# Optimization experiments

Hardware: AMD Instinct MI355X
Metric: run time of the kernel (lower is better)

The kernel has to match this reference:

```python
import jax, jax.numpy as jnp
import numpy as np

C = 640      # in_channels == out_channels (required by source: same generator applied to both)
K = 3        # kernel_size
R = int(C * 0.2)  # reduction hidden = 128
H = 10
W = 10
BS = 25      # support: 5-way 5-shot
BQ = 75      # query: 5-way 15-query


def setup_inputs() -> dict:
    key = jax.random.key(0)
    ks = jax.random.split(key, 16)
    s = 0.02  # weight scale to keep the 4-deep linear chain numerically tame
    rn = lambda k, shape: jax.random.normal(k, shape, jnp.float32) * s
    return {
        "support_set": jax.random.normal(ks[0], (BS, C, H, W), jnp.float32),
        "query_set": jax.random.normal(ks[1], (BQ, C, H, W), jnp.float32),
        # ContextLearningModule: four 1x1 convs (no nonlinearity in source)
        "Wc1": rn(ks[2], (C, C)), "bc1": jnp.zeros((C,), jnp.float32),
        "Wc2": rn(ks[3], (C, C)), "bc2": jnp.zeros((C,), jnp.float32),
        "Wc3": rn(ks[4], (C, C)), "bc3": jnp.zeros((C,), jnp.float32),
        "Wc4": rn(ks[5], (C, C)), "bc4": jnp.zeros((C,), jnp.float32),
        # DynamicKernelGenerator channel branch: Linear(C,R) -> ReLU -> Linear(R, C*K*K)
        "W1": rn(ks[6], (C, R)), "b1": jnp.zeros((R,), jnp.float32),
        "W2": rn(ks[7], (R, C * K * K)), "b2": jnp.zeros((C * K * K,), jnp.float32),
        # DynamicKernelGenerator spatial branch: Conv2d(C, K*K, 1)
        "Ws": rn(ks[8], (K * K, C)), "bs": jnp.zeros((K * K,), jnp.float32),
    }


def _conv1x1(x, Wt, b):
    # x: [b, c, h, w], Wt: [o, c]
    return jnp.einsum('bchw,oc->bohw', x, Wt) + b[None, :, None, None]


def _dyn_kernel(x, W1, b1, W2, b2, Ws, bs):
    # x: [b, C, h, w] -> per-pixel dynamic kernel [b, C, h, w, K, K]
    b, c, h, w = x.shape
    pooled = x.mean(axis=(2, 3))  # adaptive_avg_pool2d(...,1)
    ck = jax.nn.relu(pooled @ W1 + b1) @ W2 + b2          # [b, C*K*K]
    ck = ck.reshape(b, c, K, K)                            # channel kernel
    sk = jnp.einsum('bchw,kc->bkhw', x, Ws) + bs[None, :, None, None]
    sk = sk.reshape(b, h, w, K, K)                         # raw view, as in source
    return ck[:, :, None, None, :, :] * sk[:, None, :, :, :, :]


def _involution(x, kernel):
    # x: [b, C, h, w]; kernel: [b or 1, C, h, w, K, K]
    # out[b,c,i,j] = sum_{u,v} kernel[b,c,i,j,u,v] * x[b,c,i+u-p, j+v-p]
    h, w = x.shape[-2:]
    p = K // 2
    xp = jnp.pad(x, ((0, 0), (0, 0), (p, p), (p, p)))
    return sum(kernel[..., u, v] * xp[:, :, u:u + h, v:v + w]
               for u in range(K) for v in range(K))


def reference(support_set, query_set, Wc1, bc1, Wc2, bc2, Wc3, bc3, Wc4, bc4,
              W1, b1, W2, b2, Ws, bs):
    sf, qf = support_set, query_set  # identity backbone
    # context learning module
    tsr = _conv1x1(_conv1x1(_conv1x1(_conv1x1(sf, Wc1, bc1), Wc2, bc2), Wc3, bc3), Wc4, bc4)
    # task-specific kernel, averaged over the support batch -> [1, C, H, W, K, K]
    task_kernel = _dyn_kernel(tsr, W1, b1, W2, b2, Ws, bs).mean(axis=0, keepdims=True)
    # per-instance kernels (batched; identical math to the per-sample loop)
    inst_kernels = _dyn_kernel(sf, W1, b1, W2, b2, Ws, bs)  # [BS, C, H, W, K, K]
    fused = inst_kernels * task_kernel
    adapted_support = _involution(sf, fused)        # [BS, C, H, W]
    adapted_query = _involution(qf, task_kernel)    # [BQ, C, H, W] (kernel broadcast)
    return (adapted_support, adapted_query)
```

## Files before the change

kernel.cpp:

```cpp
#include <hip/hip_runtime.h>

#define CCH   640
#define RDIM  128
#define HWPIX 100
#define NBS   25
#define NBQ   75
#define CKK   5760
#define SF_B  64000

#define OFF_PG0   0
#define OFF_PGA   16000
#define OFF_PGB   32000
#define OFF_ATA   48000
#define OFF_ATB   53760
#define OFF_BA    59520
#define OFF_BB    59536
#define OFF_HP    59552
#define OFF_SKT   85152
#define OFF_SKS   130152
#define OFF_SKSCT 175152
#define OFF_CKT   197652
#define OFF_CKS   341652
#define OFF_TASKT 485652

__global__ void pool_kernel(const float* __restrict__ sf, float* __restrict__ Pg0) {
    int idx = blockIdx.x * 64 + threadIdx.x;
    if (idx >= NBS * CCH) return;
    int b = idx / CCH, c = idx % CCH;
    const float4* s4 = (const float4*)(sf + b * SF_B + c * HWPIX);
    float acc = 0.f;
#pragma unroll
    for (int q = 0; q < 25; ++q) {
        float4 v = s4[q];
        acc += (v.x + v.y) + (v.z + v.w);
    }
    Pg0[idx] = acc * 0.01f;
}

__global__ void chain_step(const float* __restrict__ Pin, const float* __restrict__ Wp,
                           const float* __restrict__ bp, float* __restrict__ Pout,
                           const float* __restrict__ Ain, const float* __restrict__ Wa,
                           const float* __restrict__ ba, const float* __restrict__ Bin,
                           float* __restrict__ Aout, float* __restrict__ Bout,
                           int first, const float* __restrict__ Ws, const float* __restrict__ bs) {
    __shared__ float red[256];
    int blk = blockIdx.x, t = threadIdx.x;
    int lane = t & 63;
    if (blk < 4000) {
        int W = blk * 4 + (t >> 6);
        int o = W / NBS, b = W % NBS;
        const float2* w2 = (const float2*)(Wp + o * CCH);
        const float2* p2 = (const float2*)(Pin + b * CCH);
        float acc = 0.f;
#pragma unroll
        for (int s = 0; s < 5; ++s) {
            float2 wv = w2[s * 64 + lane];
            float2 pv = p2[s * 64 + lane];
            acc += wv.x * pv.x + wv.y * pv.y;
        }
#pragma unroll
        for (int m = 32; m >= 1; m >>= 1) acc += __shfl_xor(acc, m);
        if (lane == 0) Pout[b * CCH + o] = acc + bp[o];
    } else if (blk < 4090) {
        int w = blk - 4000;
        int k = w / 10, ctile = w % 10;
        int og = t >> 6, cl = lane;
        int c = ctile * 64 + cl;
        int o0 = og * 160;
        float acc = 0.f;
        if (first) {
            const float* ar = Ws + k * CCH;
#pragma unroll 8
            for (int o = o0; o < o0 + 160; ++o)
                acc += ar[o] * Wa[o * CCH + c];
        } else {
#pragma unroll 8
            for (int o = o0; o < o0 + 160; ++o)
                acc += Ain[o * 9 + k] * Wa[o * CCH + c];
        }
        red[t] = acc;
        __syncthreads();
        if (t < 64) {
            float s = red[t] + red[64 + t] + red[128 + t] + red[192 + t];
            Aout[(ctile * 64 + t) * 9 + k] = s;
        }
    } else {
        int WB = (blk - 4090) * 4 + (t >> 6);
        if (WB >= 9) return;
        int k = WB;
        float acc = 0.f;
        if (first) {
            const float* ar = Ws + k * CCH;
#pragma unroll
            for (int s = 0; s < 10; ++s) acc += ar[s * 64 + lane] * ba[s * 64 + lane];
        } else {
#pragma unroll
            for (int s = 0; s < 10; ++s) acc += Ain[(s * 64 + lane) * 9 + k] * ba[s * 64 + lane];
        }
#pragma unroll
        for (int m = 32; m >= 1; m >>= 1) acc += __shfl_xor(acc, m);
        if (lane == 0) Bout[k] = acc + (first ? bs[k] : Bin[k]);
    }
}

__global__ void postchain(const float* __restrict__ sf, const float* __restrict__ Pg0,
                          const float* __restrict__ Pgf, const float* __restrict__ W1,
                          float* __restrict__ Hp, const float* __restrict__ A4T,
                          const float* __restrict__ betaF, const float* __restrict__ Ws,
                          const float* __restrict__ bs, float* __restrict__ SKT,
                          float* __restrict__ SKS) {
    int blk = blockIdx.x, t = threadIdx.x;
    if (blk < 100) {
        int pair = blk / 2;
        int s = (blk % 2) * 2 + (t >> 7);
        int r = t & 127;
        int branch = pair / NBS, b = pair % NBS;
        const float* prow = (branch ? Pg0 : Pgf) + b * CCH;
        int c0 = s * 160;
        float acc = 0.f;
#pragma unroll 8
        for (int c = 0; c < 160; ++c)
            acc += prow[c0 + c] * W1[(c0 + c) * RDIM + r];
        Hp[(pair * 4 + s) * RDIM + r] = acc;
    } else {
        int sidx = (blk - 100) * 256 + t;
        if (sidx >= 45000) return;
        int s = sidx / 22500;
        int rem = sidx % 22500;
        int b = rem / 900;
        int r2 = rem % 900;
        int k = r2 / HWPIX, q = r2 % HWPIX;
        const float* x = sf + b * SF_B + q;
        const float* wsr = Ws + k * CCH;
        int c0 = s * 320;
        float acc0 = 0.f, acc1 = 0.f;
#pragma unroll 8
        for (int c = 0; c < 320; ++c) {
            float xc = x[(c0 + c) * HWPIX];
            acc0 += A4T[(c0 + c) * 9 + k] * xc;
            acc1 += wsr[c0 + c] * xc;
        }
        if (s == 0) { acc0 += betaF[k]; acc1 += bs[k]; }
        int p = r2 / 9, uv = r2 % 9;
        int dst = s * 22500 + b * 900 + uv * 100 + p;
        SKT[dst] = acc0;
        SKS[dst] = acc1;
    }
}

__global__ void mlp_phase2(const float* __restrict__ Hp, const float* __restrict__ b1,
                           const float* __restrict__ W2, const float* __restrict__ b2,
                           float* __restrict__ ckt, float* __restrict__ cks) {
    __shared__ float hs0[RDIM], hs1[RDIM];
    int b = blockIdx.x / 9, chunk = blockIdx.x % 9;
    int t = threadIdx.x;
    if (t < RDIM) {
        const float* hp = Hp + b * 4 * RDIM;
        hs0[t] = fmaxf(b1[t] + hp[t] + hp[RDIM + t] + hp[2 * RDIM + t] + hp[3 * RDIM + t], 0.f);
    } else if (t < 2 * RDIM) {
        int r = t - RDIM;
        const float* hp = Hp + (NBS + b) * 4 * RDIM;
        hs1[r] = fmaxf(b1[r] + hp[r] + hp[RDIM + r] + hp[2 * RDIM + r] + hp[3 * RDIM + r], 0.f);
    }
    __syncthreads();
    int jbase = chunk * 640;
    float a00 = b2[jbase + t], a01 = b2[jbase + t + 320];
    float a10 = a00, a11 = a01;
#pragma unroll 4
    for (int r = 0; r < RDIM; ++r) {
        const float* wrow = W2 + r * CKK + jbase;
        float w0 = wrow[t], w1 = wrow[t + 320];
        float h0 = hs0[r], h1 = hs1[r];
        a00 += h0 * w0; a01 += h0 * w1;
        a10 += h1 * w0; a11 += h1 * w1;
    }
    float* c0 = ckt + b * CKK + jbase;
    float* c1 = cks + b * CKK + jbase;
    c0[t] = a00; c0[t + 320] = a01;
    c1[t] = a10; c1[t + 320] = a11;
}

__global__ void task_assemble(const float* __restrict__ ckt, const float* __restrict__ SKT,
                              const float* __restrict__ SKS, float* __restrict__ taskT,
                              float* __restrict__ sksT) {
    int blk = blockIdx.x, t = threadIdx.x;
    if (blk < 2250) {
        int idx = blk * 256 + t;
        int uv = idx / 64000;
        int rem = idx % 64000;
        int c = rem / 100, p = rem % 100;
        float acc = 0.f;
#pragma unroll
        for (int b = 0; b < NBS; ++b)
            acc += ckt[b * CKK + c * 9 + uv] *
                   (SKT[b * 900 + uv * 100 + p] + SKT[22500 + b * 900 + uv * 100 + p]);
        taskT[idx] = acc * 0.04f;
    } else {
        int cidx = (blk - 2250) * 256 + t;
        if (cidx >= 22500) return;
        int uv = cidx / 2500;
        int r = cidx % 2500;
        int src = (r / 100) * 900 + uv * 100 + (r % 100);
        sksT[cidx] = SKS[src] + SKS[22500 + src];
    }
}

__global__ __launch_bounds__(256) void involutions(
        const float* __restrict__ sf, const float* __restrict__ qf,
        const float* __restrict__ taskT, const float* __restrict__ cks,
        const float* __restrict__ sksT, float* __restrict__ out) {
    int idx = blockIdx.x * 256 + threadIdx.x;
    bool support = idx < NBS * SF_B;
    int b, c, p;
    const float* x;
    if (support) {
        b = idx / SF_B; int rem = idx % SF_B; c = rem / 100; p = rem % 100;
        x = sf + b * SF_B + c * 100;
    } else {
        int qidx = idx - NBS * SF_B;
        b = qidx / SF_B; int rem = qidx % SF_B; c = rem / 100; p = rem % 100;
        x = qf + b * SF_B + c * 100;
    }
    int i = p / 10, j = p % 10;
    float acc = 0.f;
#pragma unroll
    for (int u = 0; u < 3; ++u) {
        int ii = i + u - 1;
        float mrow = ((unsigned)ii < 10u) ? 1.f : 0.f;
        int ci = min(max(ii, 0), 9);
#pragma unroll
        for (int v = 0; v < 3; ++v) {
            int jj = j + v - 1;
            float m = ((unsigned)jj < 10u) ? mrow : 0.f;
            int cj = min(max(jj, 0), 9);
            float xv = x[ci * 10 + cj] * m;
            int uv = u * 3 + v;
            float w = taskT[uv * 64000 + c * 100 + p];
            if (support)
                w *= cks[b * CKK + c * 9 + uv] * sksT[uv * 2500 + b * 100 + p];
            acc += w * xv;
        }
    }
    out[idx] = acc;
}

extern "C" void kernel_launch(void* const* d_in, const int* in_sizes, int n_in,
                              void* d_out, int out_size, void* d_ws, size_t ws_size,
                              hipStream_t stream) {
    const float* sf  = (const float*)d_in[0];
    const float* qf  = (const float*)d_in[1];
    const float* Wc[4] = {(const float*)d_in[2], (const float*)d_in[4],
                          (const float*)d_in[6], (const float*)d_in[8]};
    const float* bc[4] = {(const float*)d_in[3], (const float*)d_in[5],
                          (const float*)d_in[7], (const float*)d_in[9]};
    const float* W1 = (const float*)d_in[10];
    const float* b1 = (const float*)d_in[11];
    const float* W2 = (const float*)d_in[12];
    const float* b2 = (const float*)d_in[13];
    const float* Ws = (const float*)d_in[14];
    const float* bs = (const float*)d_in[15];
    float* out = (float*)d_out;
    float* ws = (float*)d_ws;

    float* Pg0 = ws + OFF_PG0;
    float* Pga = ws + OFF_PGA;
    float* Pgb = ws + OFF_PGB;
    float* ATa = ws + OFF_ATA;
    float* ATb = ws + OFF_ATB;
    float* Ba  = ws + OFF_BA;
    float* Bb  = ws + OFF_BB;
    float* Hp  = ws + OFF_HP;
    float* SKT = ws + OFF_SKT;
    float* SKS = ws + OFF_SKS;
    float* SKsT= ws + OFF_SKSCT;
    float* CKT = ws + OFF_CKT;
    float* CKS = ws + OFF_CKS;
    float* TKT = ws + OFF_TASKT;

    pool_kernel<<<250, 64, 0, stream>>>(sf, Pg0);

    chain_step<<<4093, 256, 0, stream>>>(Pg0, Wc[0], bc[0], Pga, nullptr, Wc[3], bc[3], nullptr,
                                         ATa, Ba, 1, Ws, bs);
    chain_step<<<4093, 256, 0, stream>>>(Pga, Wc[1], bc[1], Pgb, ATa, Wc[2], bc[2], Ba,
                                         ATb, Bb, 0, Ws, bs);
    chain_step<<<4093, 256, 0, stream>>>(Pgb, Wc[2], bc[2], Pga, ATb, Wc[1], bc[1], Bb,
                                         ATa, Ba, 0, Ws, bs);
    chain_step<<<4093, 256, 0, stream>>>(Pga, Wc[3], bc[3], Pgb, ATa, Wc[0], bc[0], Ba,
                                         ATb, Bb, 0, Ws, bs);

    postchain<<<276, 256, 0, stream>>>(sf, Pg0, Pgb, W1, Hp, ATb, Bb, Ws, bs, SKT, SKS);
    mlp_phase2<<<225, 320, 0, stream>>>(Hp, b1, W2, b2, CKT, CKS);
    task_assemble<<<2338, 256, 0, stream>>>(CKT, SKT, SKS, TKT, SKsT);
    involutions<<<25000, 256, 0, stream>>>(sf, qf, TKT, CKS, SKsT, out);
}
```

Baseline: 234.5 us.

## Merge front-end kernels into one persistent kernel with grid barriers

Replaces the eight small launches (pool, four chain steps, postchain, MLP, task assembly) with one persistent 512-block kernel that moves between phases using atomic-counter grid barriers. It also restructures the work: the last P chain step overlaps with the spatial-kernel computation, and the MLP's first layer is recomputed per block instead of being staged through the Hp buffer. The goal is to cut launch overhead and the tails between dependent small kernels. The cost is spin-wait barriers, which deadlock if the 512 blocks are not all resident at once, plus fewer blocks for the large task-assembly phase and redundant W1 work (each of 450 blocks recomputes a full 640x128 matvec).

```diff
diff --git a/kernel.cpp b/kernel.cpp
--- a/kernel.cpp
+++ b/kernel.cpp
@@ -2,11 +2,10 @@
 
 #define CCH   640
 #define RDIM  128
-#define HWPIX 100
 #define NBS   25
-#define NBQ   75
 #define CKK   5760
 #define SF_B  64000
+#define NBLK  512
 
 #define OFF_PG0   0
 #define OFF_PGA   16000
@@ -15,193 +14,248 @@
 #define OFF_ATB   53760
 #define OFF_BA    59520
 #define OFF_BB    59536
-#define OFF_HP    59552
-#define OFF_SKT   85152
-#define OFF_SKS   130152
-#define OFF_SKSCT 175152
-#define OFF_CKT   197652
-#define OFF_CKS   341652
-#define OFF_TASKT 485652
-
-__global__ void pool_kernel(const float* __restrict__ sf, float* __restrict__ Pg0) {
-    int idx = blockIdx.x * 64 + threadIdx.x;
-    if (idx >= NBS * CCH) return;
-    int b = idx / CCH, c = idx % CCH;
-    const float4* s4 = (const float4*)(sf + b * SF_B + c * HWPIX);
-    float acc = 0.f;
+#define OFF_SKT   59552
+#define OFF_SKS   104552
+#define OFF_SKSCT 149552
+#define OFF_CKT   172052
+#define OFF_CKS   316052
+#define OFF_TASKT 460052
+#define OFF_BAR   2000000
+
+#define GSYNC(id) do {                                                        \
+    __syncthreads();                                                          \
+    if (t == 0) {                                                             \
+        __threadfence();                                                      \
+        unsigned prev_ = atomicAdd(&bar[(id)], 1u);                           \
+        if (prev_ != (unsigned)(NBLK - 1)) {                                  \
+            while (atomicAdd(&bar[(id)], 0u) < (unsigned)NBLK) {              \
+                for (volatile int z_ = 0; z_ < 128; ++z_) {}                  \
+            }                                                                 \
+        }                                                                     \
+        __threadfence();                                                      \
+    }                                                                         \
+    __syncthreads();                                                          \
+} while (0)
+
+#define P_STEP(Pin, Wp, bp, Pout, WG0, STR) do {                              \
+    for (int W_ = (WG0); W_ < 16000; W_ += (STR)) {                           \
+        int o_ = W_ / NBS, b_ = W_ % NBS;                                     \
+        const float2* w2_ = (const float2*)((Wp) + o_ * CCH);                 \
+        const float2* p2_ = (const float2*)((Pin) + b_ * CCH);                \
+        float acc_ = 0.f;                                                     \
+        for (int s_ = 0; s_ < 5; ++s_) {                                      \
+            float2 wv_ = w2_[s_ * 64 + lane];                                 \
+            float2 pv_ = p2_[s_ * 64 + lane];                                 \
+            acc_ += wv_.x * pv_.x + wv_.y * pv_.y;                            \
+        }                                                                     \
+        for (int m_ = 32; m_ >= 1; m_ >>= 1) acc_ += __shfl_xor(acc_, m_);    \
+        if (lane == 0) (Pout)[b_ * CCH + o_] = acc_ + (bp)[o_];               \
+    }                                                                         \
+} while (0)
+
+#define A_STEP(w, Ain, Wa, Aout) do {                                         \
+    int k_ = (w) / 10, ctile_ = (w) % 10;                                     \
+    int og_ = t >> 6, cl_ = t & 63;                                           \
+    int c_ = ctile_ * 64 + cl_;                                               \
+    int o0_ = og_ * 160;                                                      \
+    float acc_ = 0.f;                                                         \
+    for (int o_ = o0_; o_ < o0_ + 160; ++o_)                                  \
+        acc_ += (Ain)[o_ * 9 + k_] * (Wa)[o_ * CCH + c_];                     \
+    red[t] = acc_;                                                            \
+    __syncthreads();                                                          \
+    if (t < 64)                                                               \
+        (Aout)[(ctile_ * 64 + t) * 9 + k_] =                                  \
+            red[t] + red[64 + t] + red[128 + t] + red[192 + t];               \
+} while (0)
+
+#define A_STEP_FIRST(w, Wa, Aout) do {                                        \
+    int k_ = (w) / 10, ctile_ = (w) % 10;                                     \
+    int og_ = t >> 6, cl_ = t & 63;                                           \
+    int c_ = ctile_ * 64 + cl_;                                               \
+    int o0_ = og_ * 160;                                                      \
+    const float* ar_ = Ws + k_ * CCH;                                         \
+    float acc_ = 0.f;                                                         \
+    for (int o_ = o0_; o_ < o0_ + 160; ++o_)                                  \
+        acc_ += ar_[o_] * (Wa)[o_ * CCH + c_];                                \
+    red[t] = acc_;                                                            \
+    __syncthreads();                                                          \
+    if (t < 64)                                                               \
+        (Aout)[(ctile_ * 64 + t) * 9 + k_] =                                  \
+            red[t] + red[64 + t] + red[128 + t] + red[192 + t];               \
+} while (0)
+
+#define B_STEP(kidx, Ain, bvec, Bin, Bout) do {                               \
+    float acc_ = 0.f;                                                         \
+    for (int s_ = 0; s_ < 10; ++s_) {                                         \
+        int e_ = s_ * 64 + lane;                                              \
+        acc_ += (Ain)[e_ * 9 + (kidx)] * (bvec)[e_];                          \
+    }                                                                         \
+    for (int m_ = 32; m_ >= 1; m_ >>= 1) acc_ += __shfl_xor(acc_, m_);        \
+    if (lane == 0) (Bout)[(kidx)] = acc_ + (Bin)[(kidx)];                     \
+} while (0)
+
+#define B_STEP_FIRST(kidx, bvec, Bout) do {                                   \
+    const float* ar_ = Ws + (kidx) * CCH;                                     \
+    float acc_ = 0.f;                                                         \
+    for (int s_ = 0; s_ < 10; ++s_) {                                         \
+        int e_ = s_ * 64 + lane;                                              \
+        acc_ += ar_[e_] * (bvec)[e_];                                         \
+    }                                                                         \
+    for (int m_ = 32; m_ >= 1; m_ >>= 1) acc_ += __shfl_xor(acc_, m_);        \
+    if (lane == 0) (Bout)[(kidx)] = acc_ + bs[(kidx)];                        \
+} while (0)
+
+__global__ __launch_bounds__(256) void mega_front(
+        const float* __restrict__ sf,
+        const float* __restrict__ Wc1, const float* __restrict__ bc1,
+        const float* __restrict__ Wc2, const float* __restrict__ bc2,
+        const float* __restrict__ Wc3, const float* __restrict__ bc3,
+        const float* __restrict__ Wc4, const float* __restrict__ bc4,
+        const float* __restrict__ W1, const float* __restrict__ b1,
+        const float* __restrict__ W2, const float* __restrict__ b2,
+        const float* __restrict__ Ws, const float* __restrict__ bs,
+        float* __restrict__ ws) {
+    __shared__ float red[256];
+    const int blk = blockIdx.x, t = threadIdx.x;
+    const int lane = t & 63, wib = t >> 6;
+
+    float* Pg0 = ws + OFF_PG0;
+    float* Pga = ws + OFF_PGA;
+    float* Pgb = ws + OFF_PGB;
+    float* ATa = ws + OFF_ATA;
+    float* ATb = ws + OFF_ATB;
+    float* Ba  = ws + OFF_BA;
+    float* Bb  = ws + OFF_BB;
+    float* SKT = ws + OFF_SKT;
+    float* SKS = ws + OFF_SKS;
+    float* SKsT = ws + OFF_SKSCT;
+    float* CKT = ws + OFF_CKT;
+    float* CKS = ws + OFF_CKS;
+    float* TKT = ws + OFF_TASKT;
+    unsigned* bar = (unsigned*)(ws + OFF_BAR);
+
+    if (blk < 63) {
+        int idx = blk * 256 + t;
+        if (idx < NBS * CCH) {
+            int b = idx / CCH, c = idx % CCH;
+            const float4* s4 = (const float4*)(sf + b * SF_B + c * 100);
+            float acc = 0.f;
 #pragma unroll
-    for (int q = 0; q < 25; ++q) {
-        float4 v = s4[q];
-        acc += (v.x + v.y) + (v.z + v.w);
-    }
-    Pg0[idx] = acc * 0.01f;
-}
-
-__global__ void chain_step(const float* __restrict__ Pin, const float* __restrict__ Wp,
-                           const float* __restrict__ bp, float* __restrict__ Pout,
-                           const float* __restrict__ Ain, const float* __restrict__ Wa,
-                           const float* __restrict__ ba, const float* __restrict__ Bin,
-                           float* __restrict__ Aout, float* __restrict__ Bout,
-                           int first, const float* __restrict__ Ws, const float* __restrict__ bs) {
-    __shared__ float red[256];
-    int blk = blockIdx.x, t = threadIdx.x;
-    int lane = t & 63;
-    if (blk < 4000) {
-        int W = blk * 4 + (t >> 6);
-        int o = W / NBS, b = W % NBS;
-        const float2* w2 = (const float2*)(Wp + o * CCH);
-        const float2* p2 = (const float2*)(Pin + b * CCH);
-        float acc = 0.f;
-#pragma unroll
-        for (int s = 0; s < 5; ++s) {
-            float2 wv = w2[s * 64 + lane];
-            float2 pv = p2[s * 64 + lane];
-            acc += wv.x * pv.x + wv.y * pv.y;
-        }
-#pragma unroll
-        for (int m = 32; m >= 1; m >>= 1) acc += __shfl_xor(acc, m);
-        if (lane == 0) Pout[b * CCH + o] = acc + bp[o];
-    } else if (blk < 4090) {
-        int w = blk - 4000;
-        int k = w / 10, ctile = w % 10;
-        int og = t >> 6, cl = lane;
-        int c = ctile * 64 + cl;
-        int o0 = og * 160;
-        float acc = 0.f;
-        if (first) {
-            const float* ar = Ws + k * CCH;
+            for (int q = 0; q < 25; ++q) {
+                float4 v = s4[q];
+                acc += (v.x + v.y) + (v.z + v.w);
+            }
+            Pg0[idx] = acc * 0.01f;
+        }
+    } else if (blk < 153) {
+        A_STEP_FIRST(blk - 63, Wc4, ATa);
+    } else if (blk < 156) {
+        int kk = (blk - 153) * 4 + wib;
+        if (kk < 9) B_STEP_FIRST(kk, bc4, Ba);
+    }
+    GSYNC(0);
+
+    if (blk < 419) {
+        P_STEP(Pg0, Wc1, bc1, Pga, blk * 4 + wib, 1676);
+    } else if (blk < 509) {
+        A_STEP(blk - 419, ATa, Wc3, ATb);
+    } else {
+        int kk = (blk - 509) * 4 + wib;
+        if (kk < 9) B_STEP(kk, ATa, bc3, Ba, Bb);
+    }
+    GSYNC(1);
+
+    if (blk < 419) {
+        P_STEP(Pga, Wc2, bc2, Pgb, blk * 4 + wib, 1676);
+    } else if (blk < 509) {
+        A_STEP(blk - 419, ATb, Wc2, ATa);
+    } else {
+        int kk = (blk - 509) * 4 + wib;
+        if (kk < 9) B_STEP(kk, ATb, bc2, Bb, Ba);
+    }
+    GSYNC(2);
+
+    if (blk < 419) {
+        P_STEP(Pgb, Wc3, bc3, Pga, blk * 4 + wib, 1676);
+    } else if (blk < 509) {
+        A_STEP(blk - 419, ATa, Wc1, ATb);
+    } else {
+        int kk = (blk - 509) * 4 + wib;
+        if (kk < 9) B_STEP(kk, ATa, bc1, Ba, Bb);
+    }
+    GSYNC(3);
+
+    if (blk < 176) {
+        int sidx = blk * 256 + t;
+        if (sidx < 45000) {
+            int s = sidx / 22500;
+            int rem = sidx % 22500;
+            int b = rem / 900;
+            int r2 = rem % 900;
+            int k = r2 / 100, q = r2 % 100;
+            const float* x = sf + b * SF_B + q;
+            const float* wsr = Ws + k * CCH;
+            int c0 = s * 320;
+            float acc0 = 0.f, acc1 = 0.f;
 #pragma unroll 8
-            for (int o = o0; o < o0 + 160; ++o)
-                acc += ar[o] * Wa[o * CCH + c];
-        } else {
+            for (int c = 0; c < 320; ++c) {
+                float xc = x[(c0 + c) * 100];
+                acc0 += ATb[(c0 + c) * 9 + k] * xc;
+                acc1 += wsr[c0 + c] * xc;
+            }
+            if (s == 0) { acc0 += Bb[k]; acc1 += bs[k]; }
+            int p = r2 / 9, uv = r2 % 9;
+            int dst = s * 22500 + b * 900 + uv * 100 + p;
+            SKT[dst] = acc0;
+            SKS[dst] = acc1;
+        }
+    } else {
+        P_STEP(Pga, Wc4, bc4, Pgb, (blk - 176) * 4 + wib, 1344);
+    }
+    GSYNC(4);
+
+    if (blk < 450) {
+        int b = blk / 18, jc = blk % 18, jb = jc * 320;
+        {
+            int r = t & 127;
+            const float* prow = ((t < 128) ? Pgb : Pg0) + b * CCH;
+            float acc = b1[r];
 #pragma unroll 8
-            for (int o = o0; o < o0 + 160; ++o)
-                acc += Ain[o * 9 + k] * Wa[o * CCH + c];
-        }
-        red[t] = acc;
+            for (int c = 0; c < CCH; ++c) acc += prow[c] * W1[c * RDIM + r];
+            red[t] = fmaxf(acc, 0.f);
+        }
         __syncthreads();
-        if (t < 64) {
-            float s = red[t] + red[64 + t] + red[128 + t] + red[192 + t];
-            Aout[(ctile * 64 + t) * 9 + k] = s;
-        }
-    } else {
-        int WB = (blk - 4090) * 4 + (t >> 6);
-        if (WB >= 9) return;
-        int k = WB;
-        float acc = 0.f;
-        if (first) {
-            const float* ar = Ws + k * CCH;
-#pragma unroll
-            for (int s = 0; s < 10; ++s) acc += ar[s * 64 + lane] * ba[s * 64 + lane];
-        } else {
-#pragma unroll
-            for (int s = 0; s < 10; ++s) acc += Ain[(s * 64 + lane) * 9 + k] * ba[s * 64 + lane];
-        }
-#pragma unroll
-        for (int m = 32; m >= 1; m >>= 1) acc += __shfl_xor(acc, m);
-        if (lane == 0) Bout[k] = acc + (first ? bs[k] : Bin[k]);
-    }
-}
-
-__global__ void postchain(const float* __restrict__ sf, const float* __restrict__ Pg0,
-                          const float* __restrict__ Pgf, const float* __restrict__ W1,
-                          float* __restrict__ Hp, const float* __restrict__ A4T,
-                          const float* __restrict__ betaF, const float* __restrict__ Ws,
-                          const float* __restrict__ bs, float* __restrict__ SKT,
-                          float* __restrict__ SKS) {
-    int blk = blockIdx.x, t = threadIdx.x;
-    if (blk < 100) {
-        int pair = blk / 2;
-        int s = (blk % 2) * 2 + (t >> 7);
-        int r = t & 127;
-        int branch = pair / NBS, b = pair % NBS;
-        const float* prow = (branch ? Pg0 : Pgf) + b * CCH;
-        int c0 = s * 160;
-        float acc = 0.f;
-#pragma unroll 8
-        for (int c = 0; c < 160; ++c)
-            acc += prow[c0 + c] * W1[(c0 + c) * RDIM + r];
-        Hp[(pair * 4 + s) * RDIM + r] = acc;
-    } else {
-        int sidx = (blk - 100) * 256 + t;
-        if (sidx >= 45000) return;
-        int s = sidx / 22500;
-        int rem = sidx % 22500;
-        int b = rem / 900;
-        int r2 = rem % 900;
-        int k = r2 / HWPIX, q = r2 % HWPIX;
-        const float* x = sf + b * SF_B + q;
-        const float* wsr = Ws + k * CCH;
-        int c0 = s * 320;
-        float acc0 = 0.f, acc1 = 0.f;
-#pragma unroll 8
-        for (int c = 0; c < 320; ++c) {
-            float xc = x[(c0 + c) * HWPIX];
-            acc0 += A4T[(c0 + c) * 9 + k] * xc;
-            acc1 += wsr[c0 + c] * xc;
-        }
-        if (s == 0) { acc0 += betaF[k]; acc1 += bs[k]; }
-        int p = r2 / 9, uv = r2 % 9;
-        int dst = s * 22500 + b * 900 + uv * 100 + p;
-        SKT[dst] = acc0;
-        SKS[dst] = acc1;
-    }
-}
-
-__global__ void mlp_phase2(const float* __restrict__ Hp, const float* __restrict__ b1,
-                           const float* __restrict__ W2, const float* __restrict__ b2,
-                           float* __restrict__ ckt, float* __restrict__ cks) {
-    __shared__ float hs0[RDIM], hs1[RDIM];
-    int b = blockIdx.x / 9, chunk = blockIdx.x % 9;
-    int t = threadIdx.x;
-    if (t < RDIM) {
-        const float* hp = Hp + b * 4 * RDIM;
-        hs0[t] = fmaxf(b1[t] + hp[t] + hp[RDIM + t] + hp[2 * RDIM + t] + hp[3 * RDIM + t], 0.f);
-    } else if (t < 2 * RDIM) {
-        int r = t - RDIM;
-        const float* hp = Hp + (NBS + b) * 4 * RDIM;
-        hs1[r] = fmaxf(b1[r] + hp[r] + hp[RDIM + r] + hp[2 * RDIM + r] + hp[3 * RDIM + r], 0.f);
-    }
-    __syncthreads();
-    int jbase = chunk * 640;
-    float a00 = b2[jbase + t], a01 = b2[jbase + t + 320];
-    float a10 = a00, a11 = a01;
+        for (int j = jb + t; j < jb + 320; j += 256) {
+            float a0 = b2[j], a1 = b2[j];
 #pragma unroll 4
-    for (int r = 0; r < RDIM; ++r) {
-        const float* wrow = W2 + r * CKK + jbase;
-        float w0 = wrow[t], w1 = wrow[t + 320];
-        float h0 = hs0[r], h1 = hs1[r];
-        a00 += h0 * w0; a01 += h0 * w1;
-        a10 += h1 * w0; a11 += h1 * w1;
-    }
-    float* c0 = ckt + b * CKK + jbase;
-    float* c1 = cks + b * CKK + jbase;
-    c0[t] = a00; c0[t + 320] = a01;
-    c1[t] = a10; c1[t + 320] = a11;
-}
-
-__global__ void task_assemble(const float* __restrict__ ckt, const float* __restrict__ SKT,
-                              const float* __restrict__ SKS, float* __restrict__ taskT,
-                              float* __restrict__ sksT) {
-    int blk = blockIdx.x, t = threadIdx.x;
-    if (blk < 2250) {
-        int idx = blk * 256 + t;
+            for (int r = 0; r < RDIM; ++r) {
+                float w = W2[r * CKK + j];
+                a0 += red[r] * w;
+                a1 += red[128 + r] * w;
+            }
+            CKT[b * CKK + j] = a0;
+            CKS[b * CKK + j] = a1;
+        }
+    } else {
+        for (int cidx = (blk - 450) * 256 + t; cidx < 22500; cidx += 62 * 256) {
+            int uv = cidx / 2500;
+            int r = cidx % 2500;
+            int src = (r / 100) * 900 + uv * 100 + (r % 100);
+            SKsT[cidx] = SKS[src] + SKS[22500 + src];
+        }
+    }
+    GSYNC(5);
+
+    for (int idx = blk * 256 + t; idx < 576000; idx += NBLK * 256) {
         int uv = idx / 64000;
         int rem = idx % 64000;
         int c = rem / 100, p = rem % 100;
         float acc = 0.f;
 #pragma unroll
         for (int b = 0; b < NBS; ++b)
-            acc += ckt[b * CKK + c * 9 + uv] *
+            acc += CKT[b * CKK + c * 9 + uv] *
                    (SKT[b * 900 + uv * 100 + p] + SKT[22500 + b * 900 + uv * 100 + p]);
-        taskT[idx] = acc * 0.04f;
-    } else {
-        int cidx = (blk - 2250) * 256 + t;
-        if (cidx >= 22500) return;
-        int uv = cidx / 2500;
-        int r = cidx % 2500;
-        int src = (r / 100) * 900 + uv * 100 + (r % 100);
-        sksT[cidx] = SKS[src] + SKS[22500 + src];
+        TKT[idx] = acc * 0.04f;
     }
 }
 
@@ -249,10 +303,14 @@
                               hipStream_t stream) {
     const float* sf  = (const float*)d_in[0];
     const float* qf  = (const float*)d_in[1];
-    const float* Wc[4] = {(const float*)d_in[2], (const float*)d_in[4],
-                          (const float*)d_in[6], (const float*)d_in[8]};
-    const float* bc[4] = {(const float*)d_in[3], (const float*)d_in[5],
-                          (const float*)d_in[7], (const float*)d_in[9]};
+    const float* Wc1 = (const float*)d_in[2];
+    const float* bc1 = (const float*)d_in[3];
+    const float* Wc2 = (const float*)d_in[4];
+    const float* bc2 = (const float*)d_in[5];
+    const float* Wc3 = (const float*)d_in[6];
+    const float* bc3 = (const float*)d_in[7];
+    const float* Wc4 = (const float*)d_in[8];
+    const float* bc4 = (const float*)d_in[9];
     const float* W1 = (const float*)d_in[10];
     const float* b1 = (const float*)d_in[11];
     const float* W2 = (const float*)d_in[12];
@@ -262,34 +320,11 @@
     float* out = (float*)d_out;
     float* ws = (float*)d_ws;
 
-    float* Pg0 = ws + OFF_PG0;
-    float* Pga = ws + OFF_PGA;
-    float* Pgb = ws + OFF_PGB;
-    float* ATa = ws + OFF_ATA;
-    float* ATb = ws + OFF_ATB;
-    float* Ba  = ws + OFF_BA;
-    float* Bb  = ws + OFF_BB;
-    float* Hp  = ws + OFF_HP;
-    float* SKT = ws + OFF_SKT;
-    float* SKS = ws + OFF_SKS;
-    float* SKsT= ws + OFF_SKSCT;
-    float* CKT = ws + OFF_CKT;
-    float* CKS = ws + OFF_CKS;
-    float* TKT = ws + OFF_TASKT;
-
-    pool_kernel<<<250, 64, 0, stream>>>(sf, Pg0);
-
-    chain_step<<<4093, 256, 0, stream>>>(Pg0, Wc[0], bc[0], Pga, nullptr, Wc[3], bc[3], nullptr,
-                                         ATa, Ba, 1, Ws, bs);
-    chain_step<<<4093, 256, 0, stream>>>(Pga, Wc[1], bc[1], Pgb, ATa, Wc[2], bc[2], Ba,
-                                         ATb, Bb, 0, Ws, bs);
-    chain_step<<<4093, 256, 0, stream>>>(Pgb, Wc[2], bc[2], Pga, ATb, Wc[1], bc[1], Bb,
-                                         ATa, Ba, 0, Ws, bs);
-    chain_step<<<4093, 256, 0, stream>>>(Pga, Wc[3], bc[3], Pgb, ATa, Wc[0], bc[0], Ba,
-                                         ATb, Bb, 0, Ws, bs);
-
-    postchain<<<276, 256, 0, stream>>>(sf, Pg0, Pgb, W1, Hp, ATb, Bb, Ws, bs, SKT, SKS);
-    mlp_phase2<<<225, 320, 0, stream>>>(Hp, b1, W2, b2, CKT, CKS);
-    task_assemble<<<2338, 256, 0, stream>>>(CKT, SKT, SKS, TKT, SKsT);
-    involutions<<<25000, 256, 0, stream>>>(sf, qf, TKT, CKS, SKsT, out);
+    hipMemsetAsync((char*)d_ws + OFF_BAR * sizeof(float), 0, 64, stream);
+
+    mega_front<<<NBLK, 256, 0, stream>>>(sf, Wc1, bc1, Wc2, bc2, Wc3, bc3,
+                                         Wc4, bc4, W1, b1, W2, b2, Ws, bs, ws);
+
+    involutions<<<25000, 256, 0, stream>>>(sf, qf, ws + OFF_TASKT, ws + OFF_CKS,
+                                           ws + OFF_SKSCT, out);
 }
```

Result: slower. 913.8 us (+289.6%).

## Fuse channel-kernel MLP with task kernel assembly and reuse task weights across images

Applied to the files above, without the earlier changes.

Merges the channel-branch MLP and task-kernel assembly into one kernel that keeps per-block channel kernels in shared memory, removing the CKT buffer and a launch. The involution kernel now loads the nine task-kernel weights once per (channel, pixel) and loops over 25 images per thread, cutting redundant global reads and launch width. The fused kernel runs its heavy work on only 20 blocks, which risks serializing the MLP and assembly compute.

```diff
diff --git a/kernel.cpp b/kernel.cpp
--- a/kernel.cpp
+++ b/kernel.cpp
@@ -19,8 +19,7 @@
 #define OFF_SKT   85152
 #define OFF_SKS   130152
 #define OFF_SKSCT 175152
-#define OFF_CKT   197652
-#define OFF_CKS   341652
+#define OFF_CKS   316052
 #define OFF_TASKT 485652
 
 __global__ void pool_kernel(const float* __restrict__ sf, float* __restrict__ Pg0) {
@@ -148,60 +147,56 @@
     }
 }
 
-__global__ void mlp_phase2(const float* __restrict__ Hp, const float* __restrict__ b1,
-                           const float* __restrict__ W2, const float* __restrict__ b2,
-                           float* __restrict__ ckt, float* __restrict__ cks) {
-    __shared__ float hs0[RDIM], hs1[RDIM];
-    int b = blockIdx.x / 9, chunk = blockIdx.x % 9;
-    int t = threadIdx.x;
-    if (t < RDIM) {
-        const float* hp = Hp + b * 4 * RDIM;
-        hs0[t] = fmaxf(b1[t] + hp[t] + hp[RDIM + t] + hp[2 * RDIM + t] + hp[3 * RDIM + t], 0.f);
-    } else if (t < 2 * RDIM) {
-        int r = t - RDIM;
-        const float* hp = Hp + (NBS + b) * 4 * RDIM;
-        hs1[r] = fmaxf(b1[r] + hp[r] + hp[RDIM + r] + hp[2 * RDIM + r] + hp[3 * RDIM + r], 0.f);
-    }
-    __syncthreads();
-    int jbase = chunk * 640;
-    float a00 = b2[jbase + t], a01 = b2[jbase + t + 320];
-    float a10 = a00, a11 = a01;
+__global__ __launch_bounds__(256) void ck_task(
+        const float* __restrict__ Hp, const float* __restrict__ b1,
+        const float* __restrict__ W2, const float* __restrict__ b2,
+        const float* __restrict__ SKT, const float* __restrict__ SKS,
+        float* __restrict__ CKS, float* __restrict__ TKT,
+        float* __restrict__ sksT) {
+    int blk = blockIdx.x, t = threadIdx.x;
+    if (blk < 20) {
+        __shared__ float h[50 * RDIM];
+        __shared__ float ckt_l[25 * 288];
+        int c0 = blk * 32;
+        int j0 = c0 * 9;
+        for (int o = t; o < 50 * RDIM; o += 256) {
+            int pair = o >> 7, r = o & 127;
+            const float* hp = Hp + pair * 4 * RDIM;
+            float v = b1[r] + hp[r] + hp[RDIM + r] + hp[2 * RDIM + r] + hp[3 * RDIM + r];
+            h[o] = fmaxf(v, 0.f);
+        }
+        __syncthreads();
+        for (int o = t; o < 50 * 288; o += 256) {
+            int pair = o / 288, jj = o % 288;
+            int j = j0 + jj;
+            const float* hrow = h + pair * RDIM;
+            float acc = b2[j];
 #pragma unroll 4
-    for (int r = 0; r < RDIM; ++r) {
-        const float* wrow = W2 + r * CKK + jbase;
-        float w0 = wrow[t], w1 = wrow[t + 320];
-        float h0 = hs0[r], h1 = hs1[r];
-        a00 += h0 * w0; a01 += h0 * w1;
-        a10 += h1 * w0; a11 += h1 * w1;
-    }
-    float* c0 = ckt + b * CKK + jbase;
-    float* c1 = cks + b * CKK + jbase;
-    c0[t] = a00; c0[t + 320] = a01;
-    c1[t] = a10; c1[t + 320] = a11;
-}
-
-__global__ void task_assemble(const float* __restrict__ ckt, const float* __restrict__ SKT,
-                              const float* __restrict__ SKS, float* __restrict__ taskT,
-                              float* __restrict__ sksT) {
-    int blk = blockIdx.x, t = threadIdx.x;
-    if (blk < 2250) {
-        int idx = blk * 256 + t;
-        int uv = idx / 64000;
-        int rem = idx % 64000;
-        int c = rem / 100, p = rem % 100;
-        float acc = 0.f;
-#pragma unroll
-        for (int b = 0; b < NBS; ++b)
-            acc += ckt[b * CKK + c * 9 + uv] *
-                   (SKT[b * 900 + uv * 100 + p] + SKT[22500 + b * 900 + uv * 100 + p]);
-        taskT[idx] = acc * 0.04f;
+            for (int r = 0; r < RDIM; ++r)
+                acc += hrow[r] * W2[r * CKK + j];
+            if (pair < 25) ckt_l[pair * 288 + jj] = acc;
+            else           CKS[(pair - 25) * CKK + j] = acc;
+        }
+        __syncthreads();
+        for (int o = t; o < 28800; o += 256) {
+            int uv = o / 3200;
+            int rem = o % 3200;
+            int cl = rem / 100, p = rem % 100;
+            float acc = 0.f;
+#pragma unroll
+            for (int b = 0; b < NBS; ++b)
+                acc += ckt_l[b * 288 + cl * 9 + uv] *
+                       (SKT[b * 900 + uv * 100 + p] + SKT[22500 + b * 900 + uv * 100 + p]);
+            TKT[uv * 64000 + (c0 + cl) * 100 + p] = acc * 0.04f;
+        }
     } else {
-        int cidx = (blk - 2250) * 256 + t;
-        if (cidx >= 22500) return;
-        int uv = cidx / 2500;
-        int r = cidx % 2500;
-        int src = (r / 100) * 900 + uv * 100 + (r % 100);
-        sksT[cidx] = SKS[src] + SKS[22500 + src];
+        int cidx = (blk - 20) * 256 + t;
+        if (cidx < 22500) {
+            int uv = cidx / 2500;
+            int r = cidx % 2500;
+            int src = (r / 100) * 900 + uv * 100 + (r % 100);
+            sksT[cidx] = SKS[src] + SKS[22500 + src];
+        }
     }
 }
 
@@ -209,39 +204,48 @@
         const float* __restrict__ sf, const float* __restrict__ qf,
         const float* __restrict__ taskT, const float* __restrict__ cks,
         const float* __restrict__ sksT, float* __restrict__ out) {
-    int idx = blockIdx.x * 256 + threadIdx.x;
-    bool support = idx < NBS * SF_B;
-    int b, c, p;
-    const float* x;
-    if (support) {
-        b = idx / SF_B; int rem = idx % SF_B; c = rem / 100; p = rem % 100;
-        x = sf + b * SF_B + c * 100;
-    } else {
-        int qidx = idx - NBS * SF_B;
-        b = qidx / SF_B; int rem = qidx % SF_B; c = rem / 100; p = rem % 100;
-        x = qf + b * SF_B + c * 100;
-    }
+    int blk = blockIdx.x, t = threadIdx.x;
+    int g = blk / 250;
+    int cpidx = (blk % 250) * 256 + t;
+    int c = cpidx / 100, p = cpidx % 100;
     int i = p / 10, j = p % 10;
-    float acc = 0.f;
-#pragma unroll
-    for (int u = 0; u < 3; ++u) {
-        int ii = i + u - 1;
-        float mrow = ((unsigned)ii < 10u) ? 1.f : 0.f;
-        int ci = min(max(ii, 0), 9);
-#pragma unroll
-        for (int v = 0; v < 3; ++v) {
-            int jj = j + v - 1;
-            float m = ((unsigned)jj < 10u) ? mrow : 0.f;
-            int cj = min(max(jj, 0), 9);
-            float xv = x[ci * 10 + cj] * m;
-            int uv = u * 3 + v;
-            float w = taskT[uv * 64000 + c * 100 + p];
-            if (support)
-                w *= cks[b * CKK + c * 9 + uv] * sksT[uv * 2500 + b * 100 + p];
-            acc += w * xv;
-        }
-    }
-    out[idx] = acc;
+
+    float tk[9];
+#pragma unroll
+    for (int uv = 0; uv < 9; ++uv) tk[uv] = taskT[uv * 64000 + cpidx];
+
+    int im0 = g * 25;
+#pragma unroll 1
+    for (int im = im0; im < im0 + 25; ++im) {
+        bool support = im < NBS;
+        const float* x = (support ? sf + im * SF_B : qf + (im - NBS) * SF_B) + c * 100;
+        float w[9];
+        if (support) {
+#pragma unroll
+            for (int uv = 0; uv < 9; ++uv)
+                w[uv] = tk[uv] * cks[im * CKK + c * 9 + uv] *
+                        sksT[uv * 2500 + im * 100 + p];
+        } else {
+#pragma unroll
+            for (int uv = 0; uv < 9; ++uv) w[uv] = tk[uv];
+        }
+        float acc = 0.f;
+#pragma unroll
+        for (int u = 0; u < 3; ++u) {
+            int ii = i + u - 1;
+            float mrow = ((unsigned)ii < 10u) ? 1.f : 0.f;
+            int ci = min(max(ii, 0), 9);
+#pragma unroll
+            for (int v = 0; v < 3; ++v) {
+                int jj = j + v - 1;
+                float m = ((unsigned)jj < 10u) ? mrow : 0.f;
+                int cj = min(max(jj, 0), 9);
+                float xv = x[ci * 10 + cj] * m;
+                acc += w[u * 3 + v] * xv;
+            }
+        }
+        out[im * SF_B + cpidx] = acc;
+    }
 }
 
 extern "C" void kernel_launch(void* const* d_in, const int* in_sizes, int n_in,
@@ -273,7 +277,6 @@
     float* SKT = ws + OFF_SKT;
     float* SKS = ws + OFF_SKS;
     float* SKsT= ws + OFF_SKSCT;
-    float* CKT = ws + OFF_CKT;
     float* CKS = ws + OFF_CKS;
     float* TKT = ws + OFF_TASKT;
 
@@ -289,7 +292,6 @@
                                          ATb, Bb, 0, Ws, bs);
 
     postchain<<<276, 256, 0, stream>>>(sf, Pg0, Pgb, W1, Hp, ATb, Bb, Ws, bs, SKT, SKS);
-    mlp_phase2<<<225, 320, 0, stream>>>(Hp, b1, W2, b2, CKT, CKS);
-    task_assemble<<<2338, 256, 0, stream>>>(CKT, SKT, SKS, TKT, SKsT);
-    involutions<<<25000, 256, 0, stream>>>(sf, qf, TKT, CKS, SKsT, out);
-}
+    ck_task<<<108, 256, 0, stream>>>(Hp, b1, W2, b2, SKT, SKS, CKS, TKT, SKsT);
+    involutions<<<1000, 256, 0, stream>>>(sf, qf, TKT, CKS, SKsT, out);
+}
```

Measured after the change: 694.6 us. 2.96x slower.
